# Performance work log

Measured on AMD Instinct MI355X. Metric: run time of the kernel, lower is better.

The kernel has to match this reference:

```python
import jax, jax.numpy as jnp
import numpy as np

INFEATURES = 4096
OUTFEATURES = 11008
GROUP_SIZE = 128
N_GROUPS = INFEATURES // GROUP_SIZE  # 32
PACK = 8  # 32 bits / 4 bits


def _unpack_int4(packed):
    # packed: [R, C//8] int32 -> [R, C] int32 nibbles in [0, 15]
    shifts = (jnp.arange(PACK, dtype=jnp.int32) * 4)
    nib = (packed[:, :, None] >> shifts[None, None, :]) & 0xF
    return nib.reshape(packed.shape[0], packed.shape[1] * PACK)


def setup_inputs() -> dict:
    key = jax.random.key(0)
    k1, k2, k3, k4, k5 = jax.random.split(key, 5)
    x = jax.random.normal(k1, (2048, INFEATURES), dtype=jnp.float32)
    qweight = jax.random.randint(k2, (INFEATURES, OUTFEATURES // PACK), 0, 2147483647, dtype=jnp.int32)
    qzeros = jax.random.randint(k3, (N_GROUPS, OUTFEATURES // PACK), 0, 2147483647, dtype=jnp.int32)
    scales = jax.random.uniform(k4, (N_GROUPS, OUTFEATURES), minval=0.001, maxval=0.01, dtype=jnp.float32)
    bias = jax.random.normal(k5, (OUTFEATURES,), dtype=jnp.float32) * 0.01
    return {"x": x, "qweight": qweight, "qzeros": qzeros, "scales": scales, "bias": bias}


def reference(x, qweight, qzeros, scales, bias):
    # convert_from_uint4: dequantize packed int4 weight with per-group scale/zero
    w_int = _unpack_int4(qweight)                       # [in, out] int4 values
    z_int = _unpack_int4(qzeros)                        # [n_groups, out]
    dt = scales.dtype
    # broadcast group params to per-row (trivial g_idx: row i -> group i // GROUP_SIZE)
    z = jnp.repeat(z_int.astype(dt), GROUP_SIZE, axis=0)      # [in, out]
    s = jnp.repeat(scales, GROUP_SIZE, axis=0)                # [in, out]
    weight = (w_int.astype(dt) - z) * s                       # [in, out]
    out = jnp.matmul(x, weight) + bias                        # [tokens, out]
    return out
```

## Files before the change

kernel.cpp:

```cpp
#include <hip/hip_runtime.h>

typedef __bf16 bf16_t;
typedef bf16_t bf16x8 __attribute__((ext_vector_type(8)));
typedef float  floatx4 __attribute__((ext_vector_type(4)));
typedef unsigned int uint;

constexpr int Mdim = 2048;
constexpr int Kdim = 4096;
constexpr int Ndim = 11008;
constexpr int NPK  = Ndim / 8;
constexpr int SQ   = 68;
constexpr int BM = 128, BN = 128, BK = 64;
constexpr int SA = 72, SB = 72;

#define GLOAD_LDS16(g, l) \
    __builtin_amdgcn_global_load_lds((const __attribute__((address_space(1))) void*)(g), \
                                     (__attribute__((address_space(3))) void*)(l), 16, 0, 0)
#define MFMA(a, b, c) __builtin_amdgcn_mfma_f32_16x16x32_bf16((a), (b), (c), 0, 0, 0)
#define BAR()    __builtin_amdgcn_s_barrier()
#define LGKM0()  asm volatile("s_waitcnt lgkmcnt(0)" ::: "memory")
#define LGKM8()  asm volatile("s_waitcnt lgkmcnt(8)" ::: "memory")
#define VMCNT2() asm volatile("s_waitcnt vmcnt(2)" ::: "memory")
#define PRIO1()  __builtin_amdgcn_s_setprio(1)
#define PRIO0()  __builtin_amdgcn_s_setprio(0)

__global__ void xcast_kernel(const float* __restrict__ x, bf16_t* __restrict__ xb)
{
    const int i = (blockIdx.x * 256 + threadIdx.x) * 8;
    const float4 a = *(const float4*)(x + i);
    const float4 b = *(const float4*)(x + i + 4);
    bf16x8 v;
    v[0] = (bf16_t)a.x; v[1] = (bf16_t)a.y; v[2] = (bf16_t)a.z; v[3] = (bf16_t)a.w;
    v[4] = (bf16_t)b.x; v[5] = (bf16_t)b.y; v[6] = (bf16_t)b.z; v[7] = (bf16_t)b.w;
    *(bf16x8*)(xb + i) = v;
}

__global__ __launch_bounds__(256, 4)
void wdeq_kernel(const uint* __restrict__ qweight, const uint* __restrict__ qzeros,
                 const float* __restrict__ scales, bf16_t* __restrict__ wt)
{
    __shared__ uint qbuf[16 * SQ];
    const int t  = threadIdx.x;
    const int n0 = blockIdx.x * 128;
    const int k0 = blockIdx.y * 64;
    const int c0 = n0 >> 3;
    const int g  = k0 >> 7;

    const int qk  = t >> 2;
    const int qc4 = (t & 3) * 4;
    const uint4 w4 = *(const uint4*)(qweight + (size_t)(k0 + qk) * NPK + c0 + qc4);
    qbuf[(qc4 + 0) * SQ + qk] = w4.x;
    qbuf[(qc4 + 1) * SQ + qk] = w4.y;
    qbuf[(qc4 + 2) * SQ + qk] = w4.z;
    qbuf[(qc4 + 3) * SQ + qk] = w4.w;
    __syncthreads();

    const int nloc  = t & 127;
    const int khalf = t >> 7;
    const int cc    = nloc >> 3;
    const int jsh   = (nloc & 7) * 4;

    const uint  zw = qzeros[(size_t)g * NPK + c0 + cc];
    const float s  = scales[(size_t)g * Ndim + n0 + nloc];
    const float zs = (float)((zw >> jsh) & 15u) * s;
    const uint* qrow = &qbuf[cc * SQ + khalf * 32];
    bf16_t* dst = wt + (size_t)(n0 + nloc) * Kdim + k0 + khalf * 32;
#pragma unroll
    for (int j = 0; j < 4; ++j) {
        const uint4 qa = *(const uint4*)(qrow + j * 8);
        const uint4 qb = *(const uint4*)(qrow + j * 8 + 4);
        bf16x8 v;
        v[0] = (bf16_t)((float)((qa.x >> jsh) & 15u) * s - zs);
        v[1] = (bf16_t)((float)((qa.y >> jsh) & 15u) * s - zs);
        v[2] = (bf16_t)((float)((qa.z >> jsh) & 15u) * s - zs);
        v[3] = (bf16_t)((float)((qa.w >> jsh) & 15u) * s - zs);
        v[4] = (bf16_t)((float)((qb.x >> jsh) & 15u) * s - zs);
        v[5] = (bf16_t)((float)((qb.y >> jsh) & 15u) * s - zs);
        v[6] = (bf16_t)((float)((qb.z >> jsh) & 15u) * s - zs);
        v[7] = (bf16_t)((float)((qb.w >> jsh) & 15u) * s - zs);
        *(bf16x8*)(dst + j * 8) = v;
    }
}

__global__ __launch_bounds__(512, 2)
void gemm8_kernel(const bf16_t* __restrict__ xb, const bf16_t* __restrict__ wt,
                  const float* __restrict__ bias, float* __restrict__ out)
{
    __shared__ bf16_t As[2 * 16384];
    __shared__ bf16_t Bs[2 * 8192];

    const int t    = threadIdx.x;
    const int w    = t >> 6;
    const int lane = t & 63;
    const int quad = lane >> 4;
    const int l16  = lane & 15;
    const int wm   = w >> 2;
    const int wn   = w & 3;
    const int w64  = w * 64;

    const int flat = blockIdx.y * 86 + blockIdx.x;
    const int nf   = (flat & 7) * 86 + (flat >> 3);
    const int m0   = (nf / 86) * 256;
    const int n0   = (nf % 86) * 128;

    auto stageA = [&](int T, int h) {
        const int p  = T & 1;
        const int Tk = (T & 63) * 64;
#pragma unroll
        for (int l = 0; l < 2; ++l) {
            const int idx = l * 512 + w64 + lane;
            const int r   = idx >> 3;
            const int bc  = (idx & 7) ^ (r & 7);
            GLOAD_LDS16(xb + (size_t)(m0 + h * 128 + r) * Kdim + Tk + bc * 8,
                        As + (p * 16384 + h * 8192 + (l * 512 + w64) * 8));
        }
    };
    auto stageB = [&](int T) {
        const int p  = T & 1;
        const int Tk = (T & 63) * 64;
#pragma unroll
        for (int l = 0; l < 2; ++l) {
            const int idx = l * 512 + w64 + lane;
            const int r   = idx >> 3;
            const int bc  = (idx & 7) ^ (r & 7);
            GLOAD_LDS16(wt + (size_t)(n0 + r) * Kdim + Tk + bc * 8,
                        Bs + (p * 8192 + (l * 512 + w64) * 8));
        }
    };
    auto lda = [&](int p, int mt, int s) -> bf16x8 {
        const int r = mt * 16 + l16;
        return *(const bf16x8*)(As + p * 16384 + wm * 8192 + r * 64 +
                                ((s * 4 + quad) ^ (l16 & 7)) * 8);
    };
    auto ldb = [&](int p, int nt, int s) -> bf16x8 {
        const int r = wn * 32 + nt * 16 + l16;
        return *(const bf16x8*)(Bs + p * 8192 + r * 64 +
                                ((s * 4 + quad) ^ (l16 & 7)) * 8);
    };

    floatx4 acc[8][2];
#pragma unroll
    for (int i = 0; i < 8; ++i)
#pragma unroll
        for (int j = 0; j < 2; ++j)
            acc[i][j] = (floatx4){0.f, 0.f, 0.f, 0.f};

    stageA(0, 0); stageA(0, 1); stageB(0); stageB(1);
    VMCNT2(); BAR();

    bf16x8 av0[4], av1[4], bb[4];

#define MFMA16(MG)                                                         \
    PRIO1();                                                               \
    _Pragma("unroll") for (int mt = 0; mt < 4; ++mt) {                     \
        acc[(MG)*4 + mt][0] = MFMA(av0[mt], bb[0], acc[(MG)*4 + mt][0]);   \
        acc[(MG)*4 + mt][1] = MFMA(av0[mt], bb[1], acc[(MG)*4 + mt][1]);   \
    }                                                                      \
    _Pragma("unroll") for (int mt = 0; mt < 4; ++mt) {                     \
        acc[(MG)*4 + mt][0] = MFMA(av1[mt], bb[2], acc[(MG)*4 + mt][0]);   \
        acc[(MG)*4 + mt][1] = MFMA(av1[mt], bb[3], acc[(MG)*4 + mt][1]);   \
    }                                                                      \
    PRIO0();

    for (int i = 0; i < 32; ++i) {
        bb[0] = ldb(0, 0, 0); bb[1] = ldb(0, 1, 0);
        bb[2] = ldb(0, 0, 1); bb[3] = ldb(0, 1, 1);
#pragma unroll
        for (int mt = 0; mt < 4; ++mt) { av0[mt] = lda(0, mt, 0); av1[mt] = lda(0, mt, 1); }
        stageA(2 * i + 1, 0); stageA(2 * i + 1, 1);
        LGKM8();
        BAR(); LGKM0();
        MFMA16(0);
        BAR();

#pragma unroll
        for (int mt = 0; mt < 4; ++mt) { av0[mt] = lda(0, mt + 4, 0); av1[mt] = lda(0, mt + 4, 1); }
        stageB(2 * i + 2);
        VMCNT2();
        BAR(); LGKM0();
        MFMA16(1);
        BAR();

        bb[0] = ldb(1, 0, 0); bb[1] = ldb(1, 1, 0);
        bb[2] = ldb(1, 0, 1); bb[3] = ldb(1, 1, 1);
#pragma unroll
        for (int mt = 0; mt < 4; ++mt) { av0[mt] = lda(1, mt, 0); av1[mt] = lda(1, mt, 1); }
        stageA(2 * i + 2, 0); stageA(2 * i + 2, 1);
        LGKM8();
        BAR(); LGKM0();
        MFMA16(0);
        BAR();

#pragma unroll
        for (int mt = 0; mt < 4; ++mt) { av0[mt] = lda(1, mt + 4, 0); av1[mt] = lda(1, mt + 4, 1); }
        stageB(2 * i + 3);
        VMCNT2();
        BAR(); LGKM0();
        MFMA16(1);
        BAR();
    }
#undef MFMA16

#pragma unroll
    for (int nt = 0; nt < 2; ++nt) {
        const int col = n0 + wn * 32 + nt * 16 + l16;
        const float bv = bias[col];
#pragma unroll
        for (int mt = 0; mt < 8; ++mt) {
#pragma unroll
            for (int r = 0; r < 4; ++r) {
                const int row = m0 + wm * 128 + mt * 16 + quad * 4 + r;
                out[(size_t)row * Ndim + col] = acc[mt][nt][r] + bv;
            }
        }
    }
}

template <bool PRE>
__global__ __launch_bounds__(256, 3)
void qgemm_kernel(const float* __restrict__ x,
                  const bf16_t* __restrict__ xb,
                  const uint* __restrict__ qweight,
                  const uint* __restrict__ qzeros,
                  const float* __restrict__ scales,
                  const float* __restrict__ bias,
                  float* __restrict__ out)
{
    __shared__ bf16_t As[BM * SA];
    __shared__ bf16_t Bs[BN * SB];
    __shared__ uint   qbuf[16 * SQ];

    const int t  = threadIdx.x;
    const int m0 = blockIdx.y * BM;
    const int n0 = blockIdx.x * BN;
    const int c0 = n0 >> 3;

    const int wave = t >> 6;
    const int lane = t & 63;
    const int quad = lane >> 4;
    const int l16  = lane & 15;
    const int mw = (wave >> 1) * 64;
    const int nw = (wave & 1) * 64;

    floatx4 acc[4][4];
#pragma unroll
    for (int i = 0; i < 4; ++i)
#pragma unroll
        for (int j = 0; j < 4; ++j)
            acc[i][j] = (floatx4){0.f, 0.f, 0.f, 0.f};

    const int am = t >> 3;
    const int ao = t & 7;
    const int qk  = t >> 2;
    const int qc4 = (t & 3) * 4;
    const int nloc  = t & 127;
    const int khalf = t >> 7;
    const int cc    = nloc >> 3;
    const int jsh   = (nloc & 7) * 4;

    for (int kt = 0; kt < Kdim / BK; ++kt) {
        const int k0 = kt * BK;
        const int g  = k0 >> 7;

#pragma unroll
        for (int p = 0; p < 4; ++p) {
            const int m = p * 32 + am;
            if (PRE) {
                const bf16x8 v = *(const bf16x8*)(xb + (size_t)(m0 + m) * Kdim + k0 + ao * 8);
                *(bf16x8*)&As[m * SA + ao * 8] = v;
            } else {
                const float* src = x + (size_t)(m0 + m) * Kdim + k0 + ao * 8;
                const float4 a = *(const float4*)src;
                const float4 b = *(const float4*)(src + 4);
                bf16x8 v;
                v[0] = (bf16_t)a.x; v[1] = (bf16_t)a.y; v[2] = (bf16_t)a.z; v[3] = (bf16_t)a.w;
                v[4] = (bf16_t)b.x; v[5] = (bf16_t)b.y; v[6] = (bf16_t)b.z; v[7] = (bf16_t)b.w;
                *(bf16x8*)&As[m * SA + ao * 8] = v;
            }
        }
        {
            const uint4 w4 = *(const uint4*)(qweight + (size_t)(k0 + qk) * NPK + c0 + qc4);
            qbuf[(qc4 + 0) * SQ + qk] = w4.x;
            qbuf[(qc4 + 1) * SQ + qk] = w4.y;
            qbuf[(qc4 + 2) * SQ + qk] = w4.z;
            qbuf[(qc4 + 3) * SQ + qk] = w4.w;
        }
        __syncthreads();

        {
            const uint  zw = qzeros[(size_t)g * NPK + c0 + cc];
            const float s  = scales[(size_t)g * Ndim + n0 + nloc];
            const float zs = (float)((zw >> jsh) & 15u) * s;
            const uint* qrow = &qbuf[cc * SQ + khalf * 32];
#pragma unroll
            for (int j = 0; j < 4; ++j) {
                const uint4 qa = *(const uint4*)(qrow + j * 8);
                const uint4 qb = *(const uint4*)(qrow + j * 8 + 4);
                bf16x8 v;
                v[0] = (bf16_t)((float)((qa.x >> jsh) & 15u) * s - zs);
                v[1] = (bf16_t)((float)((qa.y >> jsh) & 15u) * s - zs);
                v[2] = (bf16_t)((float)((qa.z >> jsh) & 15u) * s - zs);
                v[3] = (bf16_t)((float)((qa.w >> jsh) & 15u) * s - zs);
                v[4] = (bf16_t)((float)((qb.x >> jsh) & 15u) * s - zs);
                v[5] = (bf16_t)((float)((qb.y >> jsh) & 15u) * s - zs);
                v[6] = (bf16_t)((float)((qb.z >> jsh) & 15u) * s - zs);
                v[7] = (bf16_t)((float)((qb.w >> jsh) & 15u) * s - zs);
                *(bf16x8*)&Bs[nloc * SB + khalf * 32 + j * 8] = v;
            }
        }
        __syncthreads();

#pragma unroll
        for (int s = 0; s < 2; ++s) {
            bf16x8 fa[4], fb[4];
#pragma unroll
            for (int mt = 0; mt < 4; ++mt)
                fa[mt] = *(const bf16x8*)&As[(mw + mt * 16 + l16) * SA + s * 32 + quad * 8];
#pragma unroll
            for (int nt = 0; nt < 4; ++nt)
                fb[nt] = *(const bf16x8*)&Bs[(nw + nt * 16 + l16) * SB + s * 32 + quad * 8];
#pragma unroll
            for (int mt = 0; mt < 4; ++mt)
#pragma unroll
                for (int nt = 0; nt < 4; ++nt)
                    acc[mt][nt] = MFMA(fa[mt], fb[nt], acc[mt][nt]);
        }
        __syncthreads();
    }

#pragma unroll
    for (int nt = 0; nt < 4; ++nt) {
        const int col = n0 + nw + nt * 16 + l16;
        const float b = bias[col];
#pragma unroll
        for (int mt = 0; mt < 4; ++mt) {
#pragma unroll
            for (int r = 0; r < 4; ++r) {
                const int row = m0 + mw + mt * 16 + quad * 4 + r;
                out[(size_t)row * Ndim + col] = acc[mt][nt][r] + b;
            }
        }
    }
}

extern "C" void kernel_launch(void* const* d_in, const int* in_sizes, int n_in,
                              void* d_out, int out_size, void* d_ws, size_t ws_size,
                              hipStream_t stream)
{
    const float* x        = (const float*)d_in[0];
    const uint*  qweight  = (const uint*)d_in[1];
    const uint*  qzeros   = (const uint*)d_in[2];
    const float* scales   = (const float*)d_in[3];
    const float* bias     = (const float*)d_in[4];
    float*       out      = (float*)d_out;

    const size_t wb_bytes = (size_t)Kdim * Ndim * sizeof(bf16_t);
    const size_t xb_bytes = (size_t)Mdim * Kdim * sizeof(bf16_t);

    if (ws_size >= wb_bytes + xb_bytes) {
        bf16_t* wt = (bf16_t*)d_ws;
        bf16_t* xbuf = (bf16_t*)((char*)d_ws + wb_bytes);
        wdeq_kernel<<<dim3(Ndim / 128, Kdim / 64), 256, 0, stream>>>(qweight, qzeros, scales, wt);
        xcast_kernel<<<(Mdim * Kdim) / (256 * 8), 256, 0, stream>>>(x, xbuf);
        gemm8_kernel<<<dim3(86, 8), dim3(512), 0, stream>>>(xbuf, wt, bias, out);
    } else {
        bf16_t* xbuf = (bf16_t*)d_ws;
        dim3 ggrid(Ndim / BN, Mdim / BM);
        if (ws_size >= xb_bytes) {
            xcast_kernel<<<(Mdim * Kdim) / (256 * 8), 256, 0, stream>>>(x, xbuf);
            qgemm_kernel<true><<<ggrid, dim3(256), 0, stream>>>(x, xbuf, qweight, qzeros, scales, bias, out);
        } else {
            qgemm_kernel<false><<<ggrid, dim3(256), 0, stream>>>(x, xbuf, qweight, qzeros, scales, bias, out);
        }
    }
}
```

Measured before the change: 394.1 us.

## Split GEMM K-tile across wave pairs with LDS reduction; retile dequant writes

The GEMM now splits each 64-wide K tile between pairs of waves. Each wave covers 64 columns over half of K, so it needs fewer LDS fragment loads per MFMA (4 A + 4 B for 16 MFMAs). The cost is a larger accumulator array and a cross-wave reduction through LDS in the epilogue, and the partial waitcnt before the barrier is removed. The dequant kernel remaps threads so that 8 adjacent threads write contiguous K chunks of the same output row, which coalesces the bf16 weight stores, but it now reloads zeros and scales once per iteration.

Result: slower. 512.1 us (+29.9%).

```diff
diff --git a/kernel.cpp b/kernel.cpp
--- a/kernel.cpp
+++ b/kernel.cpp
@@ -19,7 +19,6 @@
 #define MFMA(a, b, c) __builtin_amdgcn_mfma_f32_16x16x32_bf16((a), (b), (c), 0, 0, 0)
 #define BAR()    __builtin_amdgcn_s_barrier()
 #define LGKM0()  asm volatile("s_waitcnt lgkmcnt(0)" ::: "memory")
-#define LGKM8()  asm volatile("s_waitcnt lgkmcnt(8)" ::: "memory")
 #define VMCNT2() asm volatile("s_waitcnt vmcnt(2)" ::: "memory")
 #define PRIO1()  __builtin_amdgcn_s_setprio(1)
 #define PRIO0()  __builtin_amdgcn_s_setprio(0)
@@ -55,20 +54,19 @@
     qbuf[(qc4 + 3) * SQ + qk] = w4.w;
     __syncthreads();
 
-    const int nloc  = t & 127;
-    const int khalf = t >> 7;
-    const int cc    = nloc >> 3;
-    const int jsh   = (nloc & 7) * 4;
-
-    const uint  zw = qzeros[(size_t)g * NPK + c0 + cc];
-    const float s  = scales[(size_t)g * Ndim + n0 + nloc];
-    const float zs = (float)((zw >> jsh) & 15u) * s;
-    const uint* qrow = &qbuf[cc * SQ + khalf * 32];
-    bf16_t* dst = wt + (size_t)(n0 + nloc) * Kdim + k0 + khalf * 32;
+    const int kcol = t & 7;
+    const int nr   = t >> 3;
+    const int jsh  = (nr & 7) * 4;
 #pragma unroll
     for (int j = 0; j < 4; ++j) {
-        const uint4 qa = *(const uint4*)(qrow + j * 8);
-        const uint4 qb = *(const uint4*)(qrow + j * 8 + 4);
+        const int row = nr + j * 32;
+        const int cc  = row >> 3;
+        const uint  zw = qzeros[(size_t)g * NPK + c0 + cc];
+        const float s  = scales[(size_t)g * Ndim + n0 + row];
+        const float zs = (float)((zw >> jsh) & 15u) * s;
+        const uint* qrow = &qbuf[cc * SQ + kcol * 8];
+        const uint4 qa = *(const uint4*)(qrow);
+        const uint4 qb = *(const uint4*)(qrow + 4);
         bf16x8 v;
         v[0] = (bf16_t)((float)((qa.x >> jsh) & 15u) * s - zs);
         v[1] = (bf16_t)((float)((qa.y >> jsh) & 15u) * s - zs);
@@ -78,7 +76,7 @@
         v[5] = (bf16_t)((float)((qb.y >> jsh) & 15u) * s - zs);
         v[6] = (bf16_t)((float)((qb.z >> jsh) & 15u) * s - zs);
         v[7] = (bf16_t)((float)((qb.w >> jsh) & 15u) * s - zs);
-        *(bf16x8*)(dst + j * 8) = v;
+        *(bf16x8*)(wt + (size_t)(n0 + row) * Kdim + k0 + kcol * 8) = v;
     }
 }
 
@@ -95,7 +93,8 @@
     const int quad = lane >> 4;
     const int l16  = lane & 15;
     const int wm   = w >> 2;
-    const int wn   = w & 3;
+    const int wn   = (w >> 1) & 1;
+    const int wk   = w & 1;
     const int w64  = w * 64;
 
     const int flat = blockIdx.y * 86 + blockIdx.x;
@@ -127,72 +126,59 @@
                         Bs + (p * 8192 + (l * 512 + w64) * 8));
         }
     };
-    auto lda = [&](int p, int mt, int s) -> bf16x8 {
+    auto lda = [&](int p, int mt) -> bf16x8 {
         const int r = mt * 16 + l16;
         return *(const bf16x8*)(As + p * 16384 + wm * 8192 + r * 64 +
-                                ((s * 4 + quad) ^ (l16 & 7)) * 8);
+                                ((wk * 4 + quad) ^ (l16 & 7)) * 8);
     };
-    auto ldb = [&](int p, int nt, int s) -> bf16x8 {
-        const int r = wn * 32 + nt * 16 + l16;
+    auto ldb = [&](int p, int nt) -> bf16x8 {
+        const int r = wn * 64 + nt * 16 + l16;
         return *(const bf16x8*)(Bs + p * 8192 + r * 64 +
-                                ((s * 4 + quad) ^ (l16 & 7)) * 8);
+                                ((wk * 4 + quad) ^ (l16 & 7)) * 8);
     };
 
-    floatx4 acc[8][2];
+    floatx4 acc[8][4];
 #pragma unroll
     for (int i = 0; i < 8; ++i)
 #pragma unroll
-        for (int j = 0; j < 2; ++j)
+        for (int j = 0; j < 4; ++j)
             acc[i][j] = (floatx4){0.f, 0.f, 0.f, 0.f};
 
     stageA(0, 0); stageA(0, 1); stageB(0); stageB(1);
     VMCNT2(); BAR();
 
-    bf16x8 av0[4], av1[4], bb[4];
-
-#define MFMA16(MG)                                                         \
-    PRIO1();                                                               \
-    _Pragma("unroll") for (int mt = 0; mt < 4; ++mt) {                     \
-        acc[(MG)*4 + mt][0] = MFMA(av0[mt], bb[0], acc[(MG)*4 + mt][0]);   \
-        acc[(MG)*4 + mt][1] = MFMA(av0[mt], bb[1], acc[(MG)*4 + mt][1]);   \
-    }                                                                      \
-    _Pragma("unroll") for (int mt = 0; mt < 4; ++mt) {                     \
-        acc[(MG)*4 + mt][0] = MFMA(av1[mt], bb[2], acc[(MG)*4 + mt][0]);   \
-        acc[(MG)*4 + mt][1] = MFMA(av1[mt], bb[3], acc[(MG)*4 + mt][1]);   \
-    }                                                                      \
+    bf16x8 av[4], bb[4];
+
+#define MFMA16(G)                                                              \
+    PRIO1();                                                                   \
+    _Pragma("unroll") for (int mt = 0; mt < 4; ++mt)                           \
+        _Pragma("unroll") for (int nt = 0; nt < 4; ++nt)                       \
+            acc[(G)*4 + mt][nt] = MFMA(av[mt], bb[nt], acc[(G)*4 + mt][nt]);   \
     PRIO0();
 
     for (int i = 0; i < 32; ++i) {
-        bb[0] = ldb(0, 0, 0); bb[1] = ldb(0, 1, 0);
-        bb[2] = ldb(0, 0, 1); bb[3] = ldb(0, 1, 1);
-#pragma unroll
-        for (int mt = 0; mt < 4; ++mt) { av0[mt] = lda(0, mt, 0); av1[mt] = lda(0, mt, 1); }
+        bb[0] = ldb(0, 0); bb[1] = ldb(0, 1); bb[2] = ldb(0, 2); bb[3] = ldb(0, 3);
+        av[0] = lda(0, 0); av[1] = lda(0, 1); av[2] = lda(0, 2); av[3] = lda(0, 3);
         stageA(2 * i + 1, 0); stageA(2 * i + 1, 1);
-        LGKM8();
         BAR(); LGKM0();
         MFMA16(0);
         BAR();
 
-#pragma unroll
-        for (int mt = 0; mt < 4; ++mt) { av0[mt] = lda(0, mt + 4, 0); av1[mt] = lda(0, mt + 4, 1); }
+        av[0] = lda(0, 4); av[1] = lda(0, 5); av[2] = lda(0, 6); av[3] = lda(0, 7);
         stageB(2 * i + 2);
         VMCNT2();
         BAR(); LGKM0();
         MFMA16(1);
         BAR();
 
-        bb[0] = ldb(1, 0, 0); bb[1] = ldb(1, 1, 0);
-        bb[2] = ldb(1, 0, 1); bb[3] = ldb(1, 1, 1);
-#pragma unroll
-        for (int mt = 0; mt < 4; ++mt) { av0[mt] = lda(1, mt, 0); av1[mt] = lda(1, mt, 1); }
+        bb[0] = ldb(1, 0); bb[1] = ldb(1, 1); bb[2] = ldb(1, 2); bb[3] = ldb(1, 3);
+        av[0] = lda(1, 0); av[1] = lda(1, 1); av[2] = lda(1, 2); av[3] = lda(1, 3);
         stageA(2 * i + 2, 0); stageA(2 * i + 2, 1);
-        LGKM8();
         BAR(); LGKM0();
         MFMA16(0);
         BAR();
 
-#pragma unroll
-        for (int mt = 0; mt < 4; ++mt) { av0[mt] = lda(1, mt + 4, 0); av1[mt] = lda(1, mt + 4, 1); }
+        av[0] = lda(1, 4); av[1] = lda(1, 5); av[2] = lda(1, 6); av[3] = lda(1, 7);
         stageB(2 * i + 3);
         VMCNT2();
         BAR(); LGKM0();
@@ -201,12 +187,38 @@
     }
 #undef MFMA16
 
-#pragma unroll
-    for (int nt = 0; nt < 2; ++nt) {
-        const int col = n0 + wn * 32 + nt * 16 + l16;
+    {
+        float* exf = (float*)As;
+        const int pw = w ^ 1;
+#pragma unroll
+        for (int c = 0; c < 2; ++c) {
+            const int sbase = (wk ? 0 : 4) + c * 2;
+            const int kbase = (wk ? 4 : 0) + c * 2;
+#pragma unroll
+            for (int q = 0; q < 2; ++q)
+#pragma unroll
+                for (int nt = 0; nt < 4; ++nt)
+                    *(floatx4*)(exf + w * 2048 + ((q * 4 + nt) * 64 + lane) * 4) =
+                        acc[sbase + q][nt];
+            __syncthreads();
+#pragma unroll
+            for (int q = 0; q < 2; ++q)
+#pragma unroll
+                for (int nt = 0; nt < 4; ++nt)
+                    acc[kbase + q][nt] += *(const floatx4*)(exf + pw * 2048 +
+                                            ((q * 4 + nt) * 64 + lane) * 4);
+            __syncthreads();
+        }
+    }
+
+    const int mbase = wk ? 4 : 0;
+#pragma unroll
+    for (int nt = 0; nt < 4; ++nt) {
+        const int col = n0 + wn * 64 + nt * 16 + l16;
         const float bv = bias[col];
 #pragma unroll
-        for (int mt = 0; mt < 8; ++mt) {
+        for (int q = 0; q < 4; ++q) {
+            const int mt = mbase + q;
 #pragma unroll
             for (int r = 0; r < 4; ++r) {
                 const int row = m0 + wm * 128 + mt * 16 + quad * 4 + r;
```
